# Kernel optimization log

Hardware: AMD Instinct MI355X
Metric: run time of the kernel (lower is better)

Reference implementation:

```python
import jax, jax.numpy as jnp
import numpy as np
from jax import lax

ITER = 10
SMOOTH = 1.0


def _max_pool3(x):
    # 3x3 max pool, stride 1, pad 1 (torch pads with -inf for max pool)
    return lax.reduce_window(x, -np.inf, lax.max,
                             window_dimensions=(1, 1, 3, 3),
                             window_strides=(1, 1, 1, 1),
                             padding=((0, 0), (0, 0), (1, 1), (1, 1)))


def soft_skeletonize(x, thresh_width=ITER):
    def body(i, x):
        min_pool_x = -_max_pool3(-x)
        contour = jax.nn.relu(_max_pool3(min_pool_x) - min_pool_x)
        return jax.nn.relu(x - contour)
    return lax.fori_loop(0, thresh_width, body, x)


def setup_inputs() -> dict:
    key = jax.random.key(0)
    k1, k2 = jax.random.split(key)
    shape = (32, 2, 512, 512)
    y_pred = jax.random.uniform(k1, shape, dtype=jnp.float32)
    y_true = jax.random.uniform(k2, shape, dtype=jnp.float32)
    return {"y_pred": y_pred, "y_true": y_true}


def reference(y_pred, y_true):
    skel_pred = soft_skeletonize(y_pred, ITER)
    skel_true = soft_skeletonize(y_true, ITER)
    tprec = (jnp.sum((skel_pred * y_true)[:, 1:]) + SMOOTH) / (jnp.sum(skel_pred[:, 1:]) + SMOOTH)
    tsens = (jnp.sum((skel_true * y_pred)[:, 1:]) + SMOOTH) / (jnp.sum(skel_true[:, 1:]) + SMOOTH)
    cl_dice = 1.0 - 2.0 * (tprec * tsens) / (tprec + tsens)
    return cl_dice
```

## Files before the change

### kernel.cpp

```cpp
#include <hip/hip_runtime.h>

#define IMG 512
#define HW (IMG * IMG)
#define NB 32
#define NIMG 64
#define BAND 16
#define NBAND (IMG / BAND)
#define NSTG 5
#define HALO (2 * NSTG)
#define NSTEP ((BAND + 2 * HALO) / 2)
#define INF __builtin_inff()

static __device__ __forceinline__ float dpp_from_prev(float v, float ident) {
    return __int_as_float(__builtin_amdgcn_update_dpp(
        __float_as_int(ident), __float_as_int(v), 0x138, 0xF, 0xF, false));
}
static __device__ __forceinline__ float dpp_from_next(float v, float ident) {
    return __int_as_float(__builtin_amdgcn_update_dpp(
        __float_as_int(ident), __float_as_int(v), 0x130, 0xF, 0xF, false));
}

struct Row { float4 a, b; };

static __device__ __forceinline__ float min3f(float a, float b, float c) { return fminf(fminf(a, b), c); }
static __device__ __forceinline__ float max3f(float a, float b, float c) { return fmaxf(fmaxf(a, b), c); }

static __device__ __forceinline__ Row splat(float v) {
    Row r;
    r.a = make_float4(v, v, v, v);
    r.b = make_float4(v, v, v, v);
    return r;
}

static __device__ __forceinline__ Row rmin3(const Row& x, const Row& y, const Row& z) {
    Row o;
    const float* px = (const float*)&x;
    const float* py = (const float*)&y;
    const float* pz = (const float*)&z;
    float* po = (float*)&o;
#pragma unroll
    for (int i = 0; i < 8; ++i) po[i] = min3f(px[i], py[i], pz[i]);
    return o;
}

static __device__ __forceinline__ Row rmax3(const Row& x, const Row& y, const Row& z) {
    Row o;
    const float* px = (const float*)&x;
    const float* py = (const float*)&y;
    const float* pz = (const float*)&z;
    float* po = (float*)&o;
#pragma unroll
    for (int i = 0; i < 8; ++i) po[i] = max3f(px[i], py[i], pz[i]);
    return o;
}

static __device__ __forceinline__ Row hmin3(const Row& v) {
    float shl = dpp_from_prev(v.b.w, INF);
    float shr = dpp_from_next(v.a.x, INF);
    Row o;
    o.a.x = min3f(shl,   v.a.x, v.a.y);
    o.a.y = min3f(v.a.x, v.a.y, v.a.z);
    o.a.z = min3f(v.a.y, v.a.z, v.a.w);
    o.a.w = min3f(v.a.z, v.a.w, v.b.x);
    o.b.x = min3f(v.a.w, v.b.x, v.b.y);
    o.b.y = min3f(v.b.x, v.b.y, v.b.z);
    o.b.z = min3f(v.b.y, v.b.z, v.b.w);
    o.b.w = min3f(v.b.z, v.b.w, shr);
    return o;
}

static __device__ __forceinline__ Row hmax3(const Row& v) {
    float shl = dpp_from_prev(v.b.w, -INF);
    float shr = dpp_from_next(v.a.x, -INF);
    Row o;
    o.a.x = max3f(shl,   v.a.x, v.a.y);
    o.a.y = max3f(v.a.x, v.a.y, v.a.z);
    o.a.z = max3f(v.a.y, v.a.z, v.a.w);
    o.a.w = max3f(v.a.z, v.a.w, v.b.x);
    o.b.x = max3f(v.a.w, v.b.x, v.b.y);
    o.b.y = max3f(v.b.x, v.b.y, v.b.z);
    o.b.z = max3f(v.b.y, v.b.z, v.b.w);
    o.b.w = max3f(v.b.z, v.b.w, shr);
    return o;
}

template <bool EDGE>
static __device__ __forceinline__ void step2(Row (&x)[2], Row (&mn)[2],
                                             Row& in0, Row& in1, int t) {
    Row vmin0 = rmin3(x[0], x[1], in0);
    Row vmin1 = rmin3(x[1], in0, in1);
    Row mna = hmin3(vmin0);
    Row mnb = hmin3(vmin1);
    if (EDGE) {
        if ((unsigned)(t - 1) >= IMG) mna = splat(-INF);
        if ((unsigned)t >= IMG) mnb = splat(-INF);
    }
    Row vmax0 = rmax3(mn[0], mn[1], mna);
    Row vmax1 = rmax3(mn[1], mna, mnb);
    Row mp0 = hmax3(vmax0);
    Row mp1 = hmax3(vmax1);
    Row out0, out1;
    {
        const float* px0 = (const float*)&x[0];
        const float* px1 = (const float*)&x[1];
        const float* pm1 = (const float*)&mn[1];
        const float* pma = (const float*)&mna;
        const float* pp0 = (const float*)&mp0;
        const float* pp1 = (const float*)&mp1;
        float* po0 = (float*)&out0;
        float* po1 = (float*)&out1;
#pragma unroll
        for (int i = 0; i < 8; ++i) {
            po0[i] = fmaxf(px0[i] - fmaxf(pp0[i] - pm1[i], 0.f), 0.f);
            po1[i] = fmaxf(px1[i] - fmaxf(pp1[i] - pma[i], 0.f), 0.f);
        }
    }
    if (EDGE) {
        if ((unsigned)(t - 2) >= IMG) out0 = splat(INF);
        if ((unsigned)(t - 1) >= IMG) out1 = splat(INF);
    }
    x[0] = in0;  x[1] = in1;
    mn[0] = mna; mn[1] = mnb;
    in0 = out0;  in1 = out1;
}

static __device__ __forceinline__ Row load_or_inf(const float* __restrict__ p, int r, int lane) {
    if ((unsigned)r >= IMG) return splat(INF);
    const float4* q = (const float4*)(p + (size_t)r * IMG + lane * 8);
    Row o;
    o.a = q[0];
    o.b = q[1];
    return o;
}

template <bool EDGE>
static __device__ __forceinline__ void run_a(const float* __restrict__ src,
                                             float* __restrict__ dst, int B, int lane) {
    Row x[NSTG][2], mn[NSTG][2];
#pragma unroll
    for (int j = 0; j < NSTG; ++j) {
        x[j][0] = splat(INF);   x[j][1] = splat(INF);
        mn[j][0] = splat(-INF); mn[j][1] = splat(-INF);
    }
    Row pre0 = load_or_inf(src, B - HALO, lane);
    Row pre1 = load_or_inf(src, B - HALO + 1, lane);
#pragma unroll 1
    for (int k = 0; k < NSTEP; ++k) {
        const int t = B - HALO + 2 * k;
        Row in0 = pre0, in1 = pre1;
        const int tp = (k + 1 < NSTEP) ? t + 2 : -1;
        pre0 = load_or_inf(src, tp, lane);
        pre1 = load_or_inf(src, tp + 1, lane);
#pragma unroll
        for (int j = 0; j < NSTG; ++j)
            step2<EDGE>(x[j], mn[j], in0, in1, t - 2 * j);
        const int v = t - HALO;
        if ((unsigned)(v - B) < BAND) {
            float4* q0 = (float4*)(dst + (size_t)v * IMG + lane * 8);
            q0[0] = in0.a; q0[1] = in0.b;
            float4* q1 = (float4*)(dst + (size_t)(v + 1) * IMG + lane * 8);
            q1[0] = in1.a; q1[1] = in1.b;
        }
    }
}

__global__ __launch_bounds__(64, 2) void skel5_a(const float* __restrict__ yp,
                                                 const float* __restrict__ yt,
                                                 float* __restrict__ mid) {
    const int blk = blockIdx.x;
    const int img = blk >> 5, band = blk & (NBAND - 1);
    const float* src = (img < NB) ? yp + (size_t)(2 * img + 1) * HW
                                  : yt + (size_t)(2 * (img - NB) + 1) * HW;
    float* dst = mid + (size_t)img * HW;
    const int lane = threadIdx.x;
    const int B = band * BAND;
    if (band == 0 || band == NBAND - 1) run_a<true>(src, dst, B, lane);
    else                                run_a<false>(src, dst, B, lane);
}

template <bool EDGE>
static __device__ __forceinline__ void run_b(const float* __restrict__ src,
                                             const float* __restrict__ wp, int B, int lane,
                                             float& s_prod, float& s_val) {
    Row x[NSTG][2], mn[NSTG][2];
#pragma unroll
    for (int j = 0; j < NSTG; ++j) {
        x[j][0] = splat(INF);   x[j][1] = splat(INF);
        mn[j][0] = splat(-INF); mn[j][1] = splat(-INF);
    }
    Row pre0 = load_or_inf(src, B - HALO, lane);
    Row pre1 = load_or_inf(src, B - HALO + 1, lane);
#pragma unroll 1
    for (int k = 0; k < NSTEP; ++k) {
        const int t = B - HALO + 2 * k;
        Row in0 = pre0, in1 = pre1;
        const int tp = (k + 1 < NSTEP) ? t + 2 : -1;
        pre0 = load_or_inf(src, tp, lane);
        pre1 = load_or_inf(src, tp + 1, lane);
        const int v = t - HALO;
        const bool inband = (unsigned)(v - B) < BAND;
        Row w0, w1;
        if (inband) {
            const float4* q0 = (const float4*)(wp + (size_t)v * IMG + lane * 8);
            w0.a = q0[0]; w0.b = q0[1];
            const float4* q1 = (const float4*)(wp + (size_t)(v + 1) * IMG + lane * 8);
            w1.a = q1[0]; w1.b = q1[1];
        }
#pragma unroll
        for (int j = 0; j < NSTG; ++j)
            step2<EDGE>(x[j], mn[j], in0, in1, t - 2 * j);
        if (inband) {
            const float* p0 = (const float*)&in0;
            const float* p1 = (const float*)&in1;
            const float* q0 = (const float*)&w0;
            const float* q1 = (const float*)&w1;
#pragma unroll
            for (int i = 0; i < 8; ++i) {
                s_prod += p0[i] * q0[i] + p1[i] * q1[i];
                s_val += p0[i] + p1[i];
            }
        }
    }
}

__global__ __launch_bounds__(64, 2) void skel5_b(const float* __restrict__ mid,
                                                 const float* __restrict__ yp,
                                                 const float* __restrict__ yt,
                                                 double* __restrict__ acc) {
    const int blk = blockIdx.x;
    const int img = blk >> 5, band = blk & (NBAND - 1);
    const float* src = mid + (size_t)img * HW;
    const float* wp = (img < NB) ? yt + (size_t)(2 * img + 1) * HW
                                 : yp + (size_t)(2 * (img - NB) + 1) * HW;
    const int lane = threadIdx.x;
    const int B = band * BAND;

    float s_prod = 0.f, s_val = 0.f;
    if (band == 0 || band == NBAND - 1) run_b<true>(src, wp, B, lane, s_prod, s_val);
    else                                run_b<false>(src, wp, B, lane, s_prod, s_val);

#pragma unroll
    for (int off = 32; off; off >>= 1) {
        s_prod += __shfl_down(s_prod, off);
        s_val += __shfl_down(s_val, off);
    }
    if (lane == 0) {
        const int base = (img < NB) ? 0 : 2;
        atomicAdd(&acc[base], (double)s_prod);
        atomicAdd(&acc[base + 1], (double)s_val);
    }
}

__global__ void finalize(const double* __restrict__ acc, float* __restrict__ out) {
    double tprec = (acc[0] + 1.0) / (acc[1] + 1.0);
    double tsens = (acc[2] + 1.0) / (acc[3] + 1.0);
    out[0] = (float)(1.0 - 2.0 * (tprec * tsens) / (tprec + tsens));
}

extern "C" void kernel_launch(void* const* d_in, const int* in_sizes, int n_in,
                              void* d_out, int out_size, void* d_ws, size_t ws_size,
                              hipStream_t stream) {
    (void)in_sizes; (void)n_in; (void)out_size; (void)ws_size;
    const float* yp = (const float*)d_in[0];
    const float* yt = (const float*)d_in[1];
    float* out = (float*)d_out;

    float* mid = (float*)d_ws;
    double* acc = (double*)(mid + (size_t)NIMG * HW);

    hipMemsetAsync(acc, 0, 4 * sizeof(double), stream);

    const int grid = NIMG * NBAND;
    skel5_a<<<grid, 64, 0, stream>>>(yp, yt, mid);
    skel5_b<<<grid, 64, 0, stream>>>(mid, yp, yt, acc);
    finalize<<<1, 1, 0, stream>>>(acc, out);
}
```

Measured before the change: 258.8 us.

## Split skeletonization into five 2-iteration passes with smaller bands and ping-pong buffers

When the workspace is large enough, the 10 iterations are split into five kernels of 2 iterations each, ping-ponging between two workspace buffers. Bands shrink to 8 rows with a 4-row halo instead of 16 rows with a 10-row halo, and the relu step uses fmed3. The aim is to cut redundant halo recomputation and register pressure (launch bounds raised to 4 blocks per CU), in exchange for more global memory round trips and kernel launches. The old 5-iteration path is kept as a fallback for small workspaces.

```diff
diff --git a/kernel.cpp b/kernel.cpp
--- a/kernel.cpp
+++ b/kernel.cpp
@@ -4,12 +4,18 @@
 #define HW (IMG * IMG)
 #define NB 32
 #define NIMG 64
-#define BAND 16
+#define INF __builtin_inff()
+
+#define BAND 8
 #define NBAND (IMG / BAND)
+#define HALO 4
+#define NSTEP (BAND + 2 * HALO)
+
+#define FB_BAND 16
+#define FB_NBAND (IMG / FB_BAND)
 #define NSTG 5
-#define HALO (2 * NSTG)
-#define NSTEP ((BAND + 2 * HALO) / 2)
-#define INF __builtin_inff()
+#define FB_HALO (2 * NSTG)
+#define FB_NSTEP ((FB_BAND + 2 * FB_HALO) / 2)
 
 static __device__ __forceinline__ float dpp_from_prev(float v, float ident) {
     return __int_as_float(__builtin_amdgcn_update_dpp(
@@ -82,6 +88,147 @@
     o.b.z = max3f(v.b.y, v.b.z, v.b.w);
     o.b.w = max3f(v.b.z, v.b.w, shr);
     return o;
+}
+
+static __device__ __forceinline__ Row relu_out(const Row& x, const Row& mp, const Row& mn) {
+    Row o;
+    const float* px = (const float*)&x;
+    const float* pp = (const float*)&mp;
+    const float* pm = (const float*)&mn;
+    float* po = (float*)&o;
+#pragma unroll
+    for (int i = 0; i < 8; ++i) {
+        float d = pp[i] - pm[i];
+        po[i] = __builtin_amdgcn_fmed3f(0.f, px[i], px[i] - d);
+    }
+    return o;
+}
+
+static __device__ __forceinline__ Row load_row(const float* __restrict__ p, int r, int lane) {
+    if ((unsigned)r >= IMG) return splat(INF);
+    const float4* q = (const float4*)(p + (size_t)r * IMG + lane * 8);
+    Row o;
+    o.a = q[0];
+    o.b = q[1];
+    return o;
+}
+
+template <bool EDGE, int MODE>
+static __device__ __forceinline__ void run2(const float* __restrict__ src,
+                                            float* __restrict__ dst,
+                                            const float* __restrict__ w,
+                                            int B, int lane,
+                                            float& s_prod, float& s_val) {
+    Row s0x2 = splat(INF), s0x1 = splat(INF), s0m2 = splat(-INF), s0m1 = splat(-INF);
+    Row s1x2 = splat(INF), s1x1 = splat(INF), s1m2 = splat(-INF), s1m1 = splat(-INF);
+    Row pre0 = load_row(src, B - HALO, lane);
+    Row pre1 = load_row(src, B - HALO + 1, lane);
+#pragma unroll
+    for (int k = 0; k < NSTEP; ++k) {
+        const int t = B - HALO + k;
+        Row in = pre0;
+        pre0 = pre1;
+        if (k < NSTEP - 2) pre1 = load_row(src, t + 2, lane);
+        Row wrow;
+        if (MODE == 1 && k >= 8) wrow = load_row(w, t - 4, lane);
+
+        Row out0;
+        if (k >= 2) {
+            Row mnew = hmin3(rmin3(s0x2, s0x1, in));
+            if (EDGE && (unsigned)(t - 1) >= IMG) mnew = splat(-INF);
+            if (k >= 4) {
+                Row mp = hmax3(rmax3(s0m2, s0m1, mnew));
+                out0 = relu_out(s0x2, mp, s0m1);
+                if (EDGE && (unsigned)(t - 2) >= IMG) out0 = splat(INF);
+            }
+            s0m2 = s0m1; s0m1 = mnew;
+        }
+        s0x2 = s0x1; s0x1 = in;
+
+        if (k >= 4) {
+            const int u = t - 2;
+            if (k >= 6) {
+                Row mnew = hmin3(rmin3(s1x2, s1x1, out0));
+                if (EDGE && (unsigned)(u - 1) >= IMG) mnew = splat(-INF);
+                if (k >= 8) {
+                    Row mp = hmax3(rmax3(s1m2, s1m1, mnew));
+                    Row out1 = relu_out(s1x2, mp, s1m1);
+                    const int v = u - 2;
+                    if (MODE == 0) {
+                        float4* q = (float4*)(dst + (size_t)v * IMG + lane * 8);
+                        q[0] = out1.a;
+                        q[1] = out1.b;
+                    } else {
+                        const float* p = (const float*)&out1;
+                        const float* qw = (const float*)&wrow;
+#pragma unroll
+                        for (int i = 0; i < 8; ++i) {
+                            s_prod += p[i] * qw[i];
+                            s_val += p[i];
+                        }
+                    }
+                }
+                s1m2 = s1m1; s1m1 = mnew;
+            }
+            s1x2 = s1x1; s1x1 = out0;
+        }
+    }
+}
+
+__global__ __launch_bounds__(64, 4) void skel2_first(const float* __restrict__ yp,
+                                                     const float* __restrict__ yt,
+                                                     float* __restrict__ dst) {
+    const int blk = blockIdx.x;
+    const int img = blk >> 6, band = blk & (NBAND - 1);
+    const float* src = (img < NB) ? yp + (size_t)(2 * img + 1) * HW
+                                  : yt + (size_t)(2 * (img - NB) + 1) * HW;
+    float* d = dst + (size_t)img * HW;
+    const int lane = threadIdx.x;
+    const int B = band * BAND;
+    float d0 = 0.f, d1 = 0.f;
+    if (band == 0 || band == NBAND - 1) run2<true, 0>(src, d, nullptr, B, lane, d0, d1);
+    else                                run2<false, 0>(src, d, nullptr, B, lane, d0, d1);
+}
+
+__global__ __launch_bounds__(64, 4) void skel2_mid(const float* __restrict__ srcb,
+                                                   float* __restrict__ dstb) {
+    const int blk = blockIdx.x;
+    const int img = blk >> 6, band = blk & (NBAND - 1);
+    const float* src = srcb + (size_t)img * HW;
+    float* d = dstb + (size_t)img * HW;
+    const int lane = threadIdx.x;
+    const int B = band * BAND;
+    float d0 = 0.f, d1 = 0.f;
+    if (band == 0 || band == NBAND - 1) run2<true, 0>(src, d, nullptr, B, lane, d0, d1);
+    else                                run2<false, 0>(src, d, nullptr, B, lane, d0, d1);
+}
+
+__global__ __launch_bounds__(64, 4) void skel2_last(const float* __restrict__ srcb,
+                                                    const float* __restrict__ yp,
+                                                    const float* __restrict__ yt,
+                                                    double* __restrict__ acc) {
+    const int blk = blockIdx.x;
+    const int img = blk >> 6, band = blk & (NBAND - 1);
+    const float* src = srcb + (size_t)img * HW;
+    const float* w = (img < NB) ? yt + (size_t)(2 * img + 1) * HW
+                                : yp + (size_t)(2 * (img - NB) + 1) * HW;
+    const int lane = threadIdx.x;
+    const int B = band * BAND;
+
+    float s_prod = 0.f, s_val = 0.f;
+    if (band == 0 || band == NBAND - 1) run2<true, 1>(src, nullptr, w, B, lane, s_prod, s_val);
+    else                                run2<false, 1>(src, nullptr, w, B, lane, s_prod, s_val);
+
+#pragma unroll
+    for (int off = 32; off; off >>= 1) {
+        s_prod += __shfl_down(s_prod, off);
+        s_val += __shfl_down(s_val, off);
+    }
+    if (lane == 0) {
+        const int base = (img < NB) ? 0 : 2;
+        atomicAdd(&acc[base], (double)s_prod);
+        atomicAdd(&acc[base + 1], (double)s_val);
+    }
 }
 
 template <bool EDGE>
@@ -124,15 +271,6 @@
     in0 = out0;  in1 = out1;
 }
 
-static __device__ __forceinline__ Row load_or_inf(const float* __restrict__ p, int r, int lane) {
-    if ((unsigned)r >= IMG) return splat(INF);
-    const float4* q = (const float4*)(p + (size_t)r * IMG + lane * 8);
-    Row o;
-    o.a = q[0];
-    o.b = q[1];
-    return o;
-}
-
 template <bool EDGE>
 static __device__ __forceinline__ void run_a(const float* __restrict__ src,
                                              float* __restrict__ dst, int B, int lane) {
@@ -142,20 +280,20 @@
         x[j][0] = splat(INF);   x[j][1] = splat(INF);
         mn[j][0] = splat(-INF); mn[j][1] = splat(-INF);
     }
-    Row pre0 = load_or_inf(src, B - HALO, lane);
-    Row pre1 = load_or_inf(src, B - HALO + 1, lane);
+    Row pre0 = load_row(src, B - FB_HALO, lane);
+    Row pre1 = load_row(src, B - FB_HALO + 1, lane);
 #pragma unroll 1
-    for (int k = 0; k < NSTEP; ++k) {
-        const int t = B - HALO + 2 * k;
+    for (int k = 0; k < FB_NSTEP; ++k) {
+        const int t = B - FB_HALO + 2 * k;
         Row in0 = pre0, in1 = pre1;
-        const int tp = (k + 1 < NSTEP) ? t + 2 : -1;
-        pre0 = load_or_inf(src, tp, lane);
-        pre1 = load_or_inf(src, tp + 1, lane);
+        const int tp = (k + 1 < FB_NSTEP) ? t + 2 : -1;
+        pre0 = load_row(src, tp, lane);
+        pre1 = load_row(src, tp + 1, lane);
 #pragma unroll
         for (int j = 0; j < NSTG; ++j)
             step2<EDGE>(x[j], mn[j], in0, in1, t - 2 * j);
-        const int v = t - HALO;
-        if ((unsigned)(v - B) < BAND) {
+        const int v = t - FB_HALO;
+        if ((unsigned)(v - B) < FB_BAND) {
             float4* q0 = (float4*)(dst + (size_t)v * IMG + lane * 8);
             q0[0] = in0.a; q0[1] = in0.b;
             float4* q1 = (float4*)(dst + (size_t)(v + 1) * IMG + lane * 8);
@@ -168,14 +306,14 @@
                                                  const float* __restrict__ yt,
                                                  float* __restrict__ mid) {
     const int blk = blockIdx.x;
-    const int img = blk >> 5, band = blk & (NBAND - 1);
+    const int img = blk >> 5, band = blk & (FB_NBAND - 1);
     const float* src = (img < NB) ? yp + (size_t)(2 * img + 1) * HW
                                   : yt + (size_t)(2 * (img - NB) + 1) * HW;
     float* dst = mid + (size_t)img * HW;
     const int lane = threadIdx.x;
-    const int B = band * BAND;
-    if (band == 0 || band == NBAND - 1) run_a<true>(src, dst, B, lane);
-    else                                run_a<false>(src, dst, B, lane);
+    const int B = band * FB_BAND;
+    if (band == 0 || band == FB_NBAND - 1) run_a<true>(src, dst, B, lane);
+    else                                   run_a<false>(src, dst, B, lane);
 }
 
 template <bool EDGE>
@@ -188,17 +326,17 @@
         x[j][0] = splat(INF);   x[j][1] = splat(INF);
         mn[j][0] = splat(-INF); mn[j][1] = splat(-INF);
     }
-    Row pre0 = load_or_inf(src, B - HALO, lane);
-    Row pre1 = load_or_inf(src, B - HALO + 1, lane);
+    Row pre0 = load_row(src, B - FB_HALO, lane);
+    Row pre1 = load_row(src, B - FB_HALO + 1, lane);
 #pragma unroll 1
-    for (int k = 0; k < NSTEP; ++k) {
-        const int t = B - HALO + 2 * k;
+    for (int k = 0; k < FB_NSTEP; ++k) {
+        const int t = B - FB_HALO + 2 * k;
         Row in0 = pre0, in1 = pre1;
-        const int tp = (k + 1 < NSTEP) ? t + 2 : -1;
-        pre0 = load_or_inf(src, tp, lane);
-        pre1 = load_or_inf(src, tp + 1, lane);
-        const int v = t - HALO;
-        const bool inband = (unsigned)(v - B) < BAND;
+        const int tp = (k + 1 < FB_NSTEP) ? t + 2 : -1;
+        pre0 = load_row(src, tp, lane);
+        pre1 = load_row(src, tp + 1, lane);
+        const int v = t - FB_HALO;
+        const bool inband = (unsigned)(v - B) < FB_BAND;
         Row w0, w1;
         if (inband) {
             const float4* q0 = (const float4*)(wp + (size_t)v * IMG + lane * 8);
@@ -228,16 +366,16 @@
                                                  const float* __restrict__ yt,
                                                  double* __restrict__ acc) {
     const int blk = blockIdx.x;
-    const int img = blk >> 5, band = blk & (NBAND - 1);
+    const int img = blk >> 5, band = blk & (FB_NBAND - 1);
     const float* src = mid + (size_t)img * HW;
     const float* wp = (img < NB) ? yt + (size_t)(2 * img + 1) * HW
                                  : yp + (size_t)(2 * (img - NB) + 1) * HW;
     const int lane = threadIdx.x;
-    const int B = band * BAND;
+    const int B = band * FB_BAND;
 
     float s_prod = 0.f, s_val = 0.f;
-    if (band == 0 || band == NBAND - 1) run_b<true>(src, wp, B, lane, s_prod, s_val);
-    else                                run_b<false>(src, wp, B, lane, s_prod, s_val);
+    if (band == 0 || band == FB_NBAND - 1) run_b<true>(src, wp, B, lane, s_prod, s_val);
+    else                                   run_b<false>(src, wp, B, lane, s_prod, s_val);
 
 #pragma unroll
     for (int off = 32; off; off >>= 1) {
@@ -260,18 +398,37 @@
 extern "C" void kernel_launch(void* const* d_in, const int* in_sizes, int n_in,
                               void* d_out, int out_size, void* d_ws, size_t ws_size,
                               hipStream_t stream) {
-    (void)in_sizes; (void)n_in; (void)out_size; (void)ws_size;
+    (void)in_sizes; (void)n_in; (void)out_size;
     const float* yp = (const float*)d_in[0];
     const float* yt = (const float*)d_in[1];
     float* out = (float*)d_out;
 
-    float* mid = (float*)d_ws;
-    double* acc = (double*)(mid + (size_t)NIMG * HW);
-
-    hipMemsetAsync(acc, 0, 4 * sizeof(double), stream);
-
-    const int grid = NIMG * NBAND;
-    skel5_a<<<grid, 64, 0, stream>>>(yp, yt, mid);
-    skel5_b<<<grid, 64, 0, stream>>>(mid, yp, yt, acc);
-    finalize<<<1, 1, 0, stream>>>(acc, out);
-}
+    const size_t bufElems = (size_t)NIMG * HW;
+    const size_t need2 = 2 * bufElems * sizeof(float) + 4 * sizeof(double);
+
+    if (ws_size >= need2) {
+        float* bufA = (float*)d_ws;
+        float* bufB = bufA + bufElems;
+        double* acc = (double*)(bufB + bufElems);
+
+        hipMemsetAsync(acc, 0, 4 * sizeof(double), stream);
+
+        const int grid = NIMG * NBAND;
+        skel2_first<<<grid, 64, 0, stream>>>(yp, yt, bufA);
+        skel2_mid<<<grid, 64, 0, stream>>>(bufA, bufB);
+        skel2_mid<<<grid, 64, 0, stream>>>(bufB, bufA);
+        skel2_mid<<<grid, 64, 0, stream>>>(bufA, bufB);
+        skel2_last<<<grid, 64, 0, stream>>>(bufB, yp, yt, acc);
+        finalize<<<1, 1, 0, stream>>>(acc, out);
+    } else {
+        float* mid = (float*)d_ws;
+        double* acc = (double*)(mid + bufElems);
+
+        hipMemsetAsync(acc, 0, 4 * sizeof(double), stream);
+
+        const int grid = NIMG * FB_NBAND;
+        skel5_a<<<grid, 64, 0, stream>>>(yp, yt, mid);
+        skel5_b<<<grid, 64, 0, stream>>>(mid, yp, yt, acc);
+        finalize<<<1, 1, 0, stream>>>(acc, out);
+    }
+}
```

After: 437.3 us. +69.0%, slower.

## Split skeletonization into five 2-iteration passes with smaller bands

Applied to the files above, without the earlier changes.

Replaces the two fused 5-iteration kernels with five kernels of 2 iterations each, ping-ponging between two workspace buffers, and halves the band height. This cuts redundant halo recomputation and register pressure per wave, and doubles the block count. In exchange it adds three extra full-image global round trips and kernel launches. It also folds the relu/subtract into a single fmed3 per element.

```diff
diff --git a/kernel.cpp b/kernel.cpp
--- a/kernel.cpp
+++ b/kernel.cpp
@@ -4,9 +4,9 @@
 #define HW (IMG * IMG)
 #define NB 32
 #define NIMG 64
-#define BAND 16
+#define BAND 8
 #define NBAND (IMG / BAND)
-#define NSTG 5
+#define NSTG 2
 #define HALO (2 * NSTG)
 #define NSTEP ((BAND + 2 * HALO) / 2)
 #define INF __builtin_inff()
@@ -81,6 +81,29 @@
     o.b.y = max3f(v.b.x, v.b.y, v.b.z);
     o.b.z = max3f(v.b.y, v.b.z, v.b.w);
     o.b.w = max3f(v.b.z, v.b.w, shr);
+    return o;
+}
+
+static __device__ __forceinline__ Row relu_out(const Row& x, const Row& mp, const Row& mn) {
+    Row o;
+    const float* px = (const float*)&x;
+    const float* pp = (const float*)&mp;
+    const float* pm = (const float*)&mn;
+    float* po = (float*)&o;
+#pragma unroll
+    for (int i = 0; i < 8; ++i) {
+        float d = pp[i] - pm[i];
+        po[i] = __builtin_amdgcn_fmed3f(0.f, px[i], px[i] - d);
+    }
+    return o;
+}
+
+static __device__ __forceinline__ Row load_row(const float* __restrict__ p, int r, int lane) {
+    if ((unsigned)r >= IMG) return splat(INF);
+    const float4* q = (const float4*)(p + (size_t)r * IMG + lane * 8);
+    Row o;
+    o.a = q[0];
+    o.b = q[1];
     return o;
 }
 
@@ -99,22 +122,8 @@
     Row vmax1 = rmax3(mn[1], mna, mnb);
     Row mp0 = hmax3(vmax0);
     Row mp1 = hmax3(vmax1);
-    Row out0, out1;
-    {
-        const float* px0 = (const float*)&x[0];
-        const float* px1 = (const float*)&x[1];
-        const float* pm1 = (const float*)&mn[1];
-        const float* pma = (const float*)&mna;
-        const float* pp0 = (const float*)&mp0;
-        const float* pp1 = (const float*)&mp1;
-        float* po0 = (float*)&out0;
-        float* po1 = (float*)&out1;
-#pragma unroll
-        for (int i = 0; i < 8; ++i) {
-            po0[i] = fmaxf(px0[i] - fmaxf(pp0[i] - pm1[i], 0.f), 0.f);
-            po1[i] = fmaxf(px1[i] - fmaxf(pp1[i] - pma[i], 0.f), 0.f);
-        }
-    }
+    Row out0 = relu_out(x[0], mp0, mn[1]);
+    Row out1 = relu_out(x[1], mp1, mna);
     if (EDGE) {
         if ((unsigned)(t - 2) >= IMG) out0 = splat(INF);
         if ((unsigned)(t - 1) >= IMG) out1 = splat(INF);
@@ -124,83 +133,31 @@
     in0 = out0;  in1 = out1;
 }
 
-static __device__ __forceinline__ Row load_or_inf(const float* __restrict__ p, int r, int lane) {
-    if ((unsigned)r >= IMG) return splat(INF);
-    const float4* q = (const float4*)(p + (size_t)r * IMG + lane * 8);
-    Row o;
-    o.a = q[0];
-    o.b = q[1];
-    return o;
-}
-
-template <bool EDGE>
-static __device__ __forceinline__ void run_a(const float* __restrict__ src,
-                                             float* __restrict__ dst, int B, int lane) {
+template <bool EDGE, int MODE>
+static __device__ __forceinline__ void run(const float* __restrict__ src,
+                                           float* __restrict__ dst,
+                                           const float* __restrict__ wp,
+                                           int B, int lane,
+                                           float& s_prod, float& s_val) {
     Row x[NSTG][2], mn[NSTG][2];
 #pragma unroll
     for (int j = 0; j < NSTG; ++j) {
         x[j][0] = splat(INF);   x[j][1] = splat(INF);
         mn[j][0] = splat(-INF); mn[j][1] = splat(-INF);
     }
-    Row pre0 = load_or_inf(src, B - HALO, lane);
-    Row pre1 = load_or_inf(src, B - HALO + 1, lane);
+    Row pre0 = load_row(src, B - HALO, lane);
+    Row pre1 = load_row(src, B - HALO + 1, lane);
 #pragma unroll 1
     for (int k = 0; k < NSTEP; ++k) {
         const int t = B - HALO + 2 * k;
         Row in0 = pre0, in1 = pre1;
         const int tp = (k + 1 < NSTEP) ? t + 2 : -1;
-        pre0 = load_or_inf(src, tp, lane);
-        pre1 = load_or_inf(src, tp + 1, lane);
-#pragma unroll
-        for (int j = 0; j < NSTG; ++j)
-            step2<EDGE>(x[j], mn[j], in0, in1, t - 2 * j);
-        const int v = t - HALO;
-        if ((unsigned)(v - B) < BAND) {
-            float4* q0 = (float4*)(dst + (size_t)v * IMG + lane * 8);
-            q0[0] = in0.a; q0[1] = in0.b;
-            float4* q1 = (float4*)(dst + (size_t)(v + 1) * IMG + lane * 8);
-            q1[0] = in1.a; q1[1] = in1.b;
-        }
-    }
-}
-
-__global__ __launch_bounds__(64, 2) void skel5_a(const float* __restrict__ yp,
-                                                 const float* __restrict__ yt,
-                                                 float* __restrict__ mid) {
-    const int blk = blockIdx.x;
-    const int img = blk >> 5, band = blk & (NBAND - 1);
-    const float* src = (img < NB) ? yp + (size_t)(2 * img + 1) * HW
-                                  : yt + (size_t)(2 * (img - NB) + 1) * HW;
-    float* dst = mid + (size_t)img * HW;
-    const int lane = threadIdx.x;
-    const int B = band * BAND;
-    if (band == 0 || band == NBAND - 1) run_a<true>(src, dst, B, lane);
-    else                                run_a<false>(src, dst, B, lane);
-}
-
-template <bool EDGE>
-static __device__ __forceinline__ void run_b(const float* __restrict__ src,
-                                             const float* __restrict__ wp, int B, int lane,
-                                             float& s_prod, float& s_val) {
-    Row x[NSTG][2], mn[NSTG][2];
-#pragma unroll
-    for (int j = 0; j < NSTG; ++j) {
-        x[j][0] = splat(INF);   x[j][1] = splat(INF);
-        mn[j][0] = splat(-INF); mn[j][1] = splat(-INF);
-    }
-    Row pre0 = load_or_inf(src, B - HALO, lane);
-    Row pre1 = load_or_inf(src, B - HALO + 1, lane);
-#pragma unroll 1
-    for (int k = 0; k < NSTEP; ++k) {
-        const int t = B - HALO + 2 * k;
-        Row in0 = pre0, in1 = pre1;
-        const int tp = (k + 1 < NSTEP) ? t + 2 : -1;
-        pre0 = load_or_inf(src, tp, lane);
-        pre1 = load_or_inf(src, tp + 1, lane);
+        pre0 = load_row(src, tp, lane);
+        pre1 = load_row(src, tp + 1, lane);
         const int v = t - HALO;
         const bool inband = (unsigned)(v - B) < BAND;
         Row w0, w1;
-        if (inband) {
+        if (MODE == 1 && inband) {
             const float4* q0 = (const float4*)(wp + (size_t)v * IMG + lane * 8);
             w0.a = q0[0]; w0.b = q0[1];
             const float4* q1 = (const float4*)(wp + (size_t)(v + 1) * IMG + lane * 8);
@@ -210,34 +167,69 @@
         for (int j = 0; j < NSTG; ++j)
             step2<EDGE>(x[j], mn[j], in0, in1, t - 2 * j);
         if (inband) {
-            const float* p0 = (const float*)&in0;
-            const float* p1 = (const float*)&in1;
-            const float* q0 = (const float*)&w0;
-            const float* q1 = (const float*)&w1;
-#pragma unroll
-            for (int i = 0; i < 8; ++i) {
-                s_prod += p0[i] * q0[i] + p1[i] * q1[i];
-                s_val += p0[i] + p1[i];
+            if (MODE == 0) {
+                float4* q0 = (float4*)(dst + (size_t)v * IMG + lane * 8);
+                q0[0] = in0.a; q0[1] = in0.b;
+                float4* q1 = (float4*)(dst + (size_t)(v + 1) * IMG + lane * 8);
+                q1[0] = in1.a; q1[1] = in1.b;
+            } else {
+                const float* p0 = (const float*)&in0;
+                const float* p1 = (const float*)&in1;
+                const float* q0 = (const float*)&w0;
+                const float* q1 = (const float*)&w1;
+#pragma unroll
+                for (int i = 0; i < 8; ++i) {
+                    s_prod += p0[i] * q0[i] + p1[i] * q1[i];
+                    s_val += p0[i] + p1[i];
+                }
             }
         }
     }
 }
 
-__global__ __launch_bounds__(64, 2) void skel5_b(const float* __restrict__ mid,
-                                                 const float* __restrict__ yp,
-                                                 const float* __restrict__ yt,
-                                                 double* __restrict__ acc) {
+__global__ __launch_bounds__(64, 2) void skel2_first(const float* __restrict__ yp,
+                                                     const float* __restrict__ yt,
+                                                     float* __restrict__ dst) {
     const int blk = blockIdx.x;
-    const int img = blk >> 5, band = blk & (NBAND - 1);
-    const float* src = mid + (size_t)img * HW;
-    const float* wp = (img < NB) ? yt + (size_t)(2 * img + 1) * HW
-                                 : yp + (size_t)(2 * (img - NB) + 1) * HW;
+    const int img = blk >> 6, band = blk & (NBAND - 1);
+    const float* src = (img < NB) ? yp + (size_t)(2 * img + 1) * HW
+                                  : yt + (size_t)(2 * (img - NB) + 1) * HW;
+    float* d = dst + (size_t)img * HW;
     const int lane = threadIdx.x;
     const int B = band * BAND;
+    float d0 = 0.f, d1 = 0.f;
+    if (band == 0 || band == NBAND - 1) run<true, 0>(src, d, nullptr, B, lane, d0, d1);
+    else                                run<false, 0>(src, d, nullptr, B, lane, d0, d1);
+}
+
+__global__ __launch_bounds__(64, 2) void skel2_mid(const float* __restrict__ srcb,
+                                                   float* __restrict__ dstb) {
+    const int blk = blockIdx.x;
+    const int img = blk >> 6, band = blk & (NBAND - 1);
+    const float* src = srcb + (size_t)img * HW;
+    float* d = dstb + (size_t)img * HW;
+    const int lane = threadIdx.x;
+    const int B = band * BAND;
+    float d0 = 0.f, d1 = 0.f;
+    if (band == 0 || band == NBAND - 1) run<true, 0>(src, d, nullptr, B, lane, d0, d1);
+    else                                run<false, 0>(src, d, nullptr, B, lane, d0, d1);
+}
+
+__global__ __launch_bounds__(64, 2) void skel2_last(const float* __restrict__ srcb,
+                                                    const float* __restrict__ yp,
+                                                    const float* __restrict__ yt,
+                                                    double* __restrict__ acc) {
+    const int blk = blockIdx.x;
+    const int img = blk >> 6, band = blk & (NBAND - 1);
+    const float* src = srcb + (size_t)img * HW;
+    const float* w = (img < NB) ? yt + (size_t)(2 * img + 1) * HW
+                                : yp + (size_t)(2 * (img - NB) + 1) * HW;
+    const int lane = threadIdx.x;
+    const int B = band * BAND;
 
     float s_prod = 0.f, s_val = 0.f;
-    if (band == 0 || band == NBAND - 1) run_b<true>(src, wp, B, lane, s_prod, s_val);
-    else                                run_b<false>(src, wp, B, lane, s_prod, s_val);
+    if (band == 0 || band == NBAND - 1) run<true, 1>(src, nullptr, w, B, lane, s_prod, s_val);
+    else                                run<false, 1>(src, nullptr, w, B, lane, s_prod, s_val);
 
 #pragma unroll
     for (int off = 32; off; off >>= 1) {
@@ -265,13 +257,17 @@
     const float* yt = (const float*)d_in[1];
     float* out = (float*)d_out;
 
-    float* mid = (float*)d_ws;
-    double* acc = (double*)(mid + (size_t)NIMG * HW);
+    float* bufA = (float*)d_ws;
+    float* bufB = bufA + (size_t)NIMG * HW;
+    double* acc = (double*)(bufB + (size_t)NIMG * HW);
 
     hipMemsetAsync(acc, 0, 4 * sizeof(double), stream);
 
     const int grid = NIMG * NBAND;
-    skel5_a<<<grid, 64, 0, stream>>>(yp, yt, mid);
-    skel5_b<<<grid, 64, 0, stream>>>(mid, yp, yt, acc);
+    skel2_first<<<grid, 64, 0, stream>>>(yp, yt, bufA);
+    skel2_mid<<<grid, 64, 0, stream>>>(bufA, bufB);
+    skel2_mid<<<grid, 64, 0, stream>>>(bufB, bufA);
+    skel2_mid<<<grid, 64, 0, stream>>>(bufA, bufB);
+    skel2_last<<<grid, 64, 0, stream>>>(bufB, yp, yt, acc);
     finalize<<<1, 1, 0, stream>>>(acc, out);
 }
```

After: 355.2 us. 1.37x slower.
